# Performance work log

Hardware: AMD Instinct MI355X
Metric: run time of the kernel (lower is better)

The kernel has to match this reference:

```python
import jax, jax.numpy as jnp
import numpy as np

T, N = 8, 4096
F_IN, F1, F2 = 128, 128, 64


def _topk_summary(emb, p, k):
    # emb: [N, r], p: [r] random projection. Returns [r, k].
    scores = emb @ p / jnp.linalg.norm(p)            # [N]
    vals, idx = jax.lax.top_k(scores, k)             # N >= k always here
    return (emb[idx] * jnp.tanh(vals)[:, None]).T    # [r, k]


def _cell(W, U, B, prev_Q, feats, p):
    # GRU-style evolution of GCN weights. prev_Q: [r, c]; feats: [N, r].
    k = prev_Q.shape[1]
    z = _topk_summary(feats, p, k)                   # [r, c]
    wz = jnp.einsum('grs,sc->grc', W, z[None].repeat(3, 0)[0][None].squeeze(0)[None, ...].squeeze(0)[None].squeeze(0)) if False else jnp.einsum('grs,sc->grc', W, z)
    u = jax.nn.sigmoid(wz[0] + U[0] @ prev_Q + B[0])
    r = jax.nn.sigmoid(wz[1] + U[1] @ prev_Q + B[1])
    h = jnp.tanh(wz[2] + U[2] @ (r * prev_Q) + B[2])
    return (1.0 - u) * prev_Q + u * h


def _grcu(W, U, B, initW, adj, feats, ps, act):
    # Sequential weight evolution over T snapshots via scan.
    def step(Q, inp):
        a, f, p = inp
        Qn = _cell(W, U, B, Q, f, p)
        emb = act(a @ (f @ Qn))                      # [N, c]
        return Qn, emb
    _, out = jax.lax.scan(step, initW, (adj, feats, ps))
    return out                                       # [T, N, c]


def setup_inputs() -> dict:
    key = jax.random.key(0)
    ks = jax.random.split(key, 12)
    s_in = 1.0 / np.sqrt(F_IN)   # Gate init stdv (rows=128 for both layers)
    s1 = 1.0 / np.sqrt(F1)
    s2 = 1.0 / np.sqrt(F2)
    adj = jax.random.uniform(ks[0], (T, N, N), dtype=jnp.float32) / N  # ~row-normalized dense adjacency
    feats = jax.random.normal(ks[1], (T, N, F_IN), dtype=jnp.float32)
    return {
        'adj': adj,
        'feats': feats,
        'p1': jax.random.normal(ks[2], (T, F_IN), dtype=jnp.float32),
        'p2': jax.random.normal(ks[3], (T, F1), dtype=jnp.float32),
        'W1': jax.random.uniform(ks[4], (3, F_IN, F_IN), minval=-s_in, maxval=s_in, dtype=jnp.float32),
        'U1': jax.random.uniform(ks[5], (3, F_IN, F_IN), minval=-s_in, maxval=s_in, dtype=jnp.float32),
        'B1': jnp.zeros((3, F_IN, F1), dtype=jnp.float32),
        'initW1': jax.random.uniform(ks[6], (F_IN, F1), minval=-s1, maxval=s1, dtype=jnp.float32),
        'W2': jax.random.uniform(ks[7], (3, F1, F1), minval=-s1, maxval=s1, dtype=jnp.float32),
        'U2': jax.random.uniform(ks[8], (3, F1, F1), minval=-s1, maxval=s1, dtype=jnp.float32),
        'B2': jnp.zeros((3, F1, F2), dtype=jnp.float32),
        'initW2': jax.random.uniform(ks[9], (F1, F2), minval=-s2, maxval=s2, dtype=jnp.float32),
    }


def reference(adj, feats, p1, p2, W1, U1, B1, initW1, W2, U2, B2, initW2):
    h1 = _grcu(W1, U1, B1, initW1, adj, feats, p1, jax.nn.relu)   # [T, N, F1]
    h2 = _grcu(W2, U2, B2, initW2, adj, h1, p2, lambda x: x)      # [T, N, F2]
    return h2[-1]                                                 # [N, F2]
```

## Files before the change

kernel.cpp:

```cpp
#include <hip/hip_runtime.h>
#include <math.h>

#define TT 8
#define NN 4096
#define FF 128

typedef short bf16x8 __attribute__((ext_vector_type(8)));
typedef float f32x4 __attribute__((ext_vector_type(4)));

__device__ inline ushort f2bf(float f) {
  uint u = __float_as_uint(f);
  return (ushort)((u + 0x7fffu + ((u >> 16) & 1u)) >> 16);
}
__device__ inline float bf2f(ushort h) { return __uint_as_float(((uint)h) << 16); }

__device__ inline void split8(const float* v, uint4& H, uint4& L) {
  ushort h[8], l[8];
  #pragma unroll
  for (int j = 0; j < 8; ++j) {
    h[j] = f2bf(v[j]);
    l[j] = f2bf(v[j] - bf2f(h[j]));
  }
  H = make_uint4((uint)h[0] | ((uint)h[1] << 16), (uint)h[2] | ((uint)h[3] << 16),
                 (uint)h[4] | ((uint)h[5] << 16), (uint)h[6] | ((uint)h[7] << 16));
  L = make_uint4((uint)l[0] | ((uint)l[1] << 16), (uint)l[2] | ((uint)l[3] << 16),
                 (uint)l[4] | ((uint)l[5] << 16), (uint)l[6] | ((uint)l[7] << 16));
}

__global__ void norm_p_k(const float* __restrict__ p1, const float* __restrict__ p2,
                         float* __restrict__ pn1, float* __restrict__ pn2) {
  int b = blockIdx.x;
  int which = b >> 3, t = b & 7;
  const float* src = which ? p2 : p1;
  float* dst = which ? pn2 : pn1;
  int lane = threadIdx.x;
  float v0 = src[t*FF + lane];
  float v1 = src[t*FF + 64 + lane];
  float ss = v0*v0 + v1*v1;
  #pragma unroll
  for (int o = 32; o > 0; o >>= 1) ss += __shfl_xor(ss, o);
  float inv = 1.0f / sqrtf(ss);
  dst[t*FF + lane] = v0 * inv;
  dst[t*FF + 64 + lane] = v1 * inv;
}

__global__ __launch_bounds__(256)
void scores_k(const float* __restrict__ src, const float* __restrict__ pn,
              float* __restrict__ sc) {
  __shared__ float ps[FF];
  int t = blockIdx.y;
  int tid = threadIdx.x;
  if (tid < FF) ps[tid] = pn[t*FF + tid];
  __syncthreads();
  int row = blockIdx.x * 64 + (tid >> 2);
  int part = tid & 3;
  const float* rp = src + ((long)t*NN + row)*FF + part*32;
  float acc = 0.f;
  #pragma unroll
  for (int i = 0; i < 8; ++i) {
    float4 f = *reinterpret_cast<const float4*>(rp + i*4);
    const float* pp = ps + part*32 + i*4;
    acc += f.x*pp[0] + f.y*pp[1] + f.z*pp[2] + f.w*pp[3];
  }
  acc += __shfl_xor(acc, 1);
  acc += __shfl_xor(acc, 2);
  if (part == 0) sc[t*NN + row] = acc;
}

template<int K>
__global__ __launch_bounds__(1024)
void sortz_k(const float* __restrict__ sc, const float* __restrict__ src,
             float* __restrict__ z) {
  __shared__ float s[NN];
  __shared__ int  si[NN];
  __shared__ float tv[K];
  int t = blockIdx.x, tid = threadIdx.x;
  for (int i = tid; i < NN; i += 1024) { s[i] = sc[(long)t*NN + i]; si[i] = i; }
  __syncthreads();
  for (int k = 2; k <= NN; k <<= 1) {
    for (int j = k >> 1; j > 0; j >>= 1) {
      for (int i = tid; i < NN; i += 1024) {
        int l = i ^ j;
        if (l > i) {
          float a = s[i], b = s[l]; int ia = si[i], ib = si[l];
          bool dir = ((i & k) == 0);
          bool lp = (b > a) || (b == a && ib < ia);
          if (lp == dir) { s[i] = b; s[l] = a; si[i] = ib; si[l] = ia; }
        }
      }
      __syncthreads();
    }
  }
  if (tid < K) tv[tid] = tanhf(s[tid]);
  __syncthreads();
  for (int e = tid; e < FF*K; e += 1024) {
    int c = e >> 7, r = e & 127;
    z[((long)t*FF + r)*K + c] = src[((long)t*NN + si[c])*FF + r] * tv[c];
  }
}

template<int C>
__global__ __launch_bounds__(128)
void cell_k(const float* __restrict__ W, const float* __restrict__ U,
            const float* __restrict__ B, const float* __restrict__ z,
            const float* __restrict__ Qp, float* __restrict__ Qo) {
  __shared__ float zc[4][FF], qc[4][FF], rq[4][FF];
  int i = threadIdx.x;
  int j0 = blockIdx.x * 4;
  #pragma unroll
  for (int jj = 0; jj < 4; ++jj) {
    zc[jj][i] = z[i*C + j0 + jj];
    qc[jj][i] = Qp[i*C + j0 + jj];
  }
  __syncthreads();
  float a0[4] = {0,0,0,0}, a1[4] = {0,0,0,0};
  const float* W0 = W + i*FF;            const float* W1r = W + FF*FF + i*FF;
  const float* U0 = U + i*FF;            const float* U1r = U + FF*FF + i*FF;
  #pragma unroll 4
  for (int k = 0; k < FF; ++k) {
    float w0 = W0[k], w1 = W1r[k], u0 = U0[k], u1 = U1r[k];
    #pragma unroll
    for (int jj = 0; jj < 4; ++jj) {
      a0[jj] += w0*zc[jj][k] + u0*qc[jj][k];
      a1[jj] += w1*zc[jj][k] + u1*qc[jj][k];
    }
  }
  float uu[4];
  #pragma unroll
  for (int jj = 0; jj < 4; ++jj) {
    float xu = a0[jj] + B[0*FF*C + i*C + j0+jj];
    uu[jj] = 1.0f / (1.0f + expf(-xu));
    float xr = a1[jj] + B[1*FF*C + i*C + j0+jj];
    float r = 1.0f / (1.0f + expf(-xr));
    rq[jj][i] = r * qc[jj][i];
  }
  __syncthreads();
  float ah[4] = {0,0,0,0};
  const float* W2 = W + 2*FF*FF + i*FF;  const float* U2 = U + 2*FF*FF + i*FF;
  #pragma unroll 4
  for (int k = 0; k < FF; ++k) {
    float w2 = W2[k], u2 = U2[k];
    #pragma unroll
    for (int jj = 0; jj < 4; ++jj) ah[jj] += w2*zc[jj][k] + u2*rq[jj][k];
  }
  #pragma unroll
  for (int jj = 0; jj < 4; ++jj) {
    float h = tanhf(ah[jj] + B[2*FF*C + i*C + j0+jj]);
    float q = qc[jj][i];
    Qo[i*C + j0+jj] = (1.0f - uu[jj])*q + uu[jj]*h;
  }
}

__global__ __launch_bounds__(256)
void xmul_pack_k(const float* __restrict__ in, const float* __restrict__ Q,
                 ushort* __restrict__ Bph, ushort* __restrict__ Bpl) {
  constexpr int C = 128, RPT = 16;
  __shared__ float Qs[64*C];
  __shared__ float ft[FF][36];
  int t = blockIdx.y;
  const float* inT = in + (long)t*NN*FF;
  const float* QT  = Q  + (long)t*128*128;
  int tid = threadIdx.x;
  int r0 = blockIdx.x * 32;
  for (int v = tid; v < 32*FF/4; v += 256) {
    int row = v >> 5, kq = v & 31;
    float4 f = *reinterpret_cast<const float4*>(inT + ((long)(r0+row))*FF + kq*4);
    ft[kq*4+0][row] = f.x; ft[kq*4+1][row] = f.y;
    ft[kq*4+2][row] = f.z; ft[kq*4+3][row] = f.w;
  }
  int c = tid & (C-1);
  int rh = tid / C;
  float acc[RPT];
  #pragma unroll
  for (int r = 0; r < RPT; ++r) acc[r] = 0.f;
  for (int kc = 0; kc < 2; ++kc) {
    __syncthreads();
    for (int v = tid*4; v < 64*C; v += 1024)
      *reinterpret_cast<float4*>(&Qs[v]) =
        *reinterpret_cast<const float4*>(QT + kc*64*C + v);
    __syncthreads();
    #pragma unroll 8
    for (int kl = 0; kl < 64; ++kl) {
      int k = kc*64 + kl;
      float qv = Qs[kl*C + c];
      const float* fr = &ft[k][rh*RPT];
      #pragma unroll
      for (int r4 = 0; r4 < RPT/4; ++r4) {
        float4 fv = *reinterpret_cast<const float4*>(fr + r4*4);
        acc[r4*4+0] += fv.x*qv; acc[r4*4+1] += fv.y*qv;
        acc[r4*4+2] += fv.z*qv; acc[r4*4+3] += fv.w*qv;
      }
    }
  }
  #pragma unroll
  for (int g = 0; g < 2; ++g) {
    uint4 H, L;
    split8(&acc[g*8], H, L);
    long k0 = r0 + rh*16 + g*8;
    long off = ((long)t*512*128 + (k0 >> 3)*128 + c)*8;
    *reinterpret_cast<uint4*>(&Bph[off]) = H;
    *reinterpret_cast<uint4*>(&Bpl[off]) = L;
  }
}

__global__ __launch_bounds__(256)
void xmul_k64(const float* __restrict__ in, const float* __restrict__ Q,
              float* __restrict__ out) {
  constexpr int C = 64, RPT = 8;
  __shared__ float Qs[64*C];
  __shared__ float ft[FF][36];
  const float* inT = in;
  const float* QT  = Q;
  int tid = threadIdx.x;
  int r0 = blockIdx.x * 32;
  for (int v = tid; v < 32*FF/4; v += 256) {
    int row = v >> 5, kq = v & 31;
    float4 f = *reinterpret_cast<const float4*>(inT + ((long)(r0+row))*FF + kq*4);
    ft[kq*4+0][row] = f.x; ft[kq*4+1][row] = f.y;
    ft[kq*4+2][row] = f.z; ft[kq*4+3][row] = f.w;
  }
  int c = tid & (C-1);
  int rh = tid / C;
  float acc[RPT];
  #pragma unroll
  for (int r = 0; r < RPT; ++r) acc[r] = 0.f;
  for (int kc = 0; kc < 2; ++kc) {
    __syncthreads();
    for (int v = tid*4; v < 64*C; v += 1024)
      *reinterpret_cast<float4*>(&Qs[v]) =
        *reinterpret_cast<const float4*>(QT + kc*64*C + v);
    __syncthreads();
    #pragma unroll 8
    for (int kl = 0; kl < 64; ++kl) {
      int k = kc*64 + kl;
      float qv = Qs[kl*C + c];
      const float* fr = &ft[k][rh*RPT];
      #pragma unroll
      for (int r4 = 0; r4 < RPT/4; ++r4) {
        float4 fv = *reinterpret_cast<const float4*>(fr + r4*4);
        acc[r4*4+0] += fv.x*qv; acc[r4*4+1] += fv.y*qv;
        acc[r4*4+2] += fv.z*qv; acc[r4*4+3] += fv.w*qv;
      }
    }
  }
  #pragma unroll
  for (int r = 0; r < RPT; ++r)
    out[((long)(r0 + rh*RPT + r))*C + c] = acc[r];
}

#define ASTRIDE 40

__global__ __launch_bounds__(256, 2)
void gemm_mfma_k(const float* __restrict__ A, const ushort* __restrict__ Bph,
                 const ushort* __restrict__ Bpl, float* __restrict__ H) {
  __shared__ ushort AsH[2][64*ASTRIDE];
  __shared__ ushort AsL[2][64*ASTRIDE];
  int bid = blockIdx.x;
  int t = bid & 7, mb = bid >> 3;
  const float* At = A + (size_t)t*NN*NN + (size_t)mb*64*NN;
  const ushort* BhT = Bph + (size_t)t*512*128*8;
  const ushort* BlT = Bpl + (size_t)t*512*128*8;
  float* Ht = H + (size_t)t*NN*FF + (size_t)mb*64*FF;

  int tid = threadIdx.x;
  int wave = tid >> 6, lane = tid & 63;
  int lg = lane >> 4, lr = lane & 15;

  int srow = tid >> 2, skq = tid & 3;
  const float* aLoad = At + (size_t)srow*NN + skq*8;
  int sOff = srow*ASTRIDE + skq*8;

  int fOff = (16*wave + lr)*ASTRIDE + lg*8;

  size_t bOff = (size_t)lg*1024 + (size_t)lr*8;

  f32x4 acc[8];
  #pragma unroll
  for (int n = 0; n < 8; ++n) acc[n] = (f32x4){0.f, 0.f, 0.f, 0.f};

  {
    float4 a0 = *reinterpret_cast<const float4*>(aLoad);
    float4 a1 = *reinterpret_cast<const float4*>(aLoad + 4);
    float v[8] = {a0.x,a0.y,a0.z,a0.w,a1.x,a1.y,a1.z,a1.w};
    uint4 Hh, Ll; split8(v, Hh, Ll);
    *reinterpret_cast<uint4*>(&AsH[0][sOff]) = Hh;
    *reinterpret_cast<uint4*>(&AsL[0][sOff]) = Ll;
  }
  __syncthreads();

  for (int s = 0; s < 128; ++s) {
    int cur = s & 1;
    float4 a0, a1;
    if (s < 127) {
      a0 = *reinterpret_cast<const float4*>(aLoad + (s+1)*32);
      a1 = *reinterpret_cast<const float4*>(aLoad + (s+1)*32 + 4);
    }
    const ushort* bh = BhT + (size_t)s*4096 + bOff;
    const ushort* bl = BlT + (size_t)s*4096 + bOff;
    bf16x8 ah = *reinterpret_cast<const bf16x8*>(&AsH[cur][fOff]);
    bf16x8 al = *reinterpret_cast<const bf16x8*>(&AsL[cur][fOff]);
    #pragma unroll
    for (int n = 0; n < 8; ++n) {
      bf16x8 bhf = *reinterpret_cast<const bf16x8*>(bh + n*128);
      bf16x8 blf = *reinterpret_cast<const bf16x8*>(bl + n*128);
      acc[n] = __builtin_amdgcn_mfma_f32_16x16x32_bf16(ah, bhf, acc[n], 0, 0, 0);
      acc[n] = __builtin_amdgcn_mfma_f32_16x16x32_bf16(al, bhf, acc[n], 0, 0, 0);
      acc[n] = __builtin_amdgcn_mfma_f32_16x16x32_bf16(ah, blf, acc[n], 0, 0, 0);
    }
    if (s < 127) {
      float v[8] = {a0.x,a0.y,a0.z,a0.w,a1.x,a1.y,a1.z,a1.w};
      uint4 Hh, Ll; split8(v, Hh, Ll);
      *reinterpret_cast<uint4*>(&AsH[cur^1][sOff]) = Hh;
      *reinterpret_cast<uint4*>(&AsL[cur^1][sOff]) = Ll;
    }
    __syncthreads();
  }

  #pragma unroll
  for (int n = 0; n < 8; ++n)
    #pragma unroll
    for (int v = 0; v < 4; ++v)
      Ht[(size_t)(16*wave + lg*4 + v)*FF + 16*n + lr] = fmaxf(acc[n][v], 0.f);
}

__global__ __launch_bounds__(256, 2)
void gemm_adj64_k(const float* __restrict__ A, const float* __restrict__ X,
                  float* __restrict__ C_) {
  constexpr int BM = 64, KB = 32, BN = 64, TN = 4, XROW = 72;
  __shared__ float As[KB][BM+4];
  __shared__ float Xs[KB*XROW];
  const float* At = A;
  const float* Xt = X;
  float* Ct = C_;
  int brow = blockIdx.x * BM;
  int tid = threadIdx.x;
  int tr = tid >> 4, tc = tid & 15;
  int arow = tid & 63, aq = tid >> 6;
  int xkk = tid >> 3;
  int xcg = (tid & 7) * 8;

  float acc[4][TN];
  #pragma unroll
  for (int i = 0; i < 4; ++i)
    #pragma unroll
    for (int j = 0; j < TN; ++j) acc[i][j] = 0.f;

  float4 ar0, ar1, xr0, xr1;
  const float* aBase = At + ((long)(brow + arow))*NN;

  auto loadG = [&](int k0) {
    ar0 = *reinterpret_cast<const float4*>(aBase + k0 + aq*8);
    ar1 = *reinterpret_cast<const float4*>(aBase + k0 + aq*8 + 4);
    const float* xp = Xt + ((long)(k0 + xkk))*BN + xcg;
    xr0 = *reinterpret_cast<const float4*>(xp);
    xr1 = *reinterpret_cast<const float4*>(xp + 4);
  };
  auto storeL = [&]() {
    As[aq*8+0][arow] = ar0.x; As[aq*8+1][arow] = ar0.y;
    As[aq*8+2][arow] = ar0.z; As[aq*8+3][arow] = ar0.w;
    As[aq*8+4][arow] = ar1.x; As[aq*8+5][arow] = ar1.y;
    As[aq*8+6][arow] = ar1.z; As[aq*8+7][arow] = ar1.w;
    int base = xkk*XROW + xcg;
    *reinterpret_cast<float4*>(&Xs[base+0]) = xr0;
    *reinterpret_cast<float4*>(&Xs[base+4]) = xr1;
  };
  auto compute = [&]() {
    #pragma unroll 8
    for (int kk = 0; kk < KB; ++kk) {
      float4 av = *reinterpret_cast<const float4*>(&As[kk][tr*4]);
      float4 b0 = *reinterpret_cast<const float4*>(&Xs[kk*XROW + tc*4]);
      float xv[TN] = {b0.x, b0.y, b0.z, b0.w};
      float am[4] = {av.x, av.y, av.z, av.w};
      #pragma unroll
      for (int i = 0; i < 4; ++i)
        #pragma unroll
        for (int j = 0; j < TN; ++j)
          acc[i][j] += am[i]*xv[j];
    }
  };

  loadG(0);
  storeL();
  __syncthreads();
  for (int ch = 1; ch < NN/KB; ++ch) {
    loadG(ch*KB);
    compute();
    __syncthreads();
    storeL();
    __syncthreads();
  }
  compute();

  #pragma unroll
  for (int i = 0; i < 4; ++i) {
    int row = brow + tr*4 + i;
    float* op = Ct + (long)row*BN + tc*TN;
    float4 o;
    o.x = acc[i][0]; o.y = acc[i][1]; o.z = acc[i][2]; o.w = acc[i][3];
    *reinterpret_cast<float4*>(op) = o;
  }
}

extern "C" void kernel_launch(void* const* d_in, const int* in_sizes, int n_in,
                              void* d_out, int out_size, void* d_ws, size_t ws_size,
                              hipStream_t stream) {
  (void)in_sizes; (void)n_in; (void)out_size; (void)ws_size;
  const float* adj   = (const float*)d_in[0];
  const float* feats = (const float*)d_in[1];
  const float* p1    = (const float*)d_in[2];
  const float* p2    = (const float*)d_in[3];
  const float* W1    = (const float*)d_in[4];
  const float* U1    = (const float*)d_in[5];
  const float* B1    = (const float*)d_in[6];
  const float* iW1   = (const float*)d_in[7];
  const float* W2    = (const float*)d_in[8];
  const float* U2    = (const float*)d_in[9];
  const float* B2    = (const float*)d_in[10];
  const float* iW2   = (const float*)d_in[11];
  float* out = (float*)d_out;
  float* ws  = (float*)d_ws;

  const long NF = (long)NN*FF;
  ushort* Bph = (ushort*)ws;
  ushort* Bpl = (ushort*)(ws + 2097152);
  float* h1  = ws + 4194304;
  float* sc  = ws + 8388608;
  float* pn1 = ws + 8421376;
  float* pn2 = ws + 8422400;
  float* z1  = ws + 8423424;
  float* z2  = ws + 8554496;
  float* Q1  = ws + 8620032;
  float* Q2  = ws + 8751104;
  float* Y   = ws + 8816640;

  norm_p_k<<<16, 64, 0, stream>>>(p1, p2, pn1, pn2);

  scores_k<<<dim3(64,8), 256, 0, stream>>>(feats, pn1, sc);
  sortz_k<128><<<8, 1024, 0, stream>>>(sc, feats, z1);
  for (int t = 0; t < TT; ++t)
    cell_k<128><<<32, 128, 0, stream>>>(W1, U1, B1, z1 + (long)t*128*128,
                                        t ? Q1 + (long)(t-1)*128*128 : iW1,
                                        Q1 + (long)t*128*128);
  xmul_pack_k<<<dim3(128,8), 256, 0, stream>>>(feats, Q1, Bph, Bpl);
  gemm_mfma_k<<<512, 256, 0, stream>>>(adj, Bph, Bpl, h1);

  scores_k<<<dim3(64,8), 256, 0, stream>>>(h1, pn2, sc);
  sortz_k<64><<<8, 1024, 0, stream>>>(sc, h1, z2);
  for (int t = 0; t < TT; ++t)
    cell_k<64><<<16, 128, 0, stream>>>(W2, U2, B2, z2 + (long)t*128*64,
                                       t ? Q2 + (long)(t-1)*128*64 : iW2,
                                       Q2 + (long)t*128*64);
  xmul_k64<<<128, 256, 0, stream>>>(h1 + 7*NF, Q2 + (long)7*128*64, Y);
  gemm_adj64_k<<<64, 256, 0, stream>>>(adj + (long)7*NN*NN, Y, out);
}
```

Baseline: 1.715 ms.

## Fuse GRU cell steps into one kernel and use MFMA for final adjacency GEMM

```diff
diff --git a/kernel.cpp b/kernel.cpp
--- a/kernel.cpp
+++ b/kernel.cpp
@@ -99,67 +99,86 @@
   }
 }
 
+template<int C, bool WRITEALL>
+__global__ __launch_bounds__(256)
+void cells_k(const float* __restrict__ W, const float* __restrict__ U,
+             const float* __restrict__ B, const float* __restrict__ z,
+             const float* __restrict__ Q0, float* __restrict__ Qout) {
+  __shared__ float zc[128][16], Qc[128][16], rq[128][16];
+  int tid = threadIdx.x;
+  int jj = tid & 15, ig = tid >> 4;
+  int j0 = blockIdx.x * 16;
+  #pragma unroll
+  for (int p = 0; p < 8; ++p) {
+    int e = p*256 + tid; int i = e >> 4, c = e & 15;
+    Qc[i][c] = Q0[i*C + j0 + c];
+  }
+  __syncthreads();
+  for (int t = 0; t < TT; ++t) {
+    #pragma unroll
+    for (int p = 0; p < 8; ++p) {
+      int e = p*256 + tid; int i = e >> 4, c = e & 15;
+      zc[i][c] = z[((long)t*128 + i)*C + j0 + c];
+    }
+    __syncthreads();
+    float uu[8];
+    #pragma unroll
+    for (int rr = 0; rr < 8; ++rr) {
+      int i = ig*8 + rr;
+      float a0 = B[(0*128 + i)*C + j0 + jj];
+      float a1 = B[(1*128 + i)*C + j0 + jj];
+      const float* W0 = W + i*128;
+      const float* W1 = W + 128*128 + i*128;
+      const float* U0 = U + i*128;
+      const float* U1 = U + 128*128 + i*128;
+      #pragma unroll 4
+      for (int k = 0; k < 128; ++k) {
+        float zv = zc[k][jj], qv = Qc[k][jj];
+        a0 += W0[k]*zv + U0[k]*qv;
+        a1 += W1[k]*zv + U1[k]*qv;
+      }
+      float uv = 1.0f / (1.0f + expf(-a0));
+      float rv = 1.0f / (1.0f + expf(-a1));
+      uu[rr] = uv;
+      rq[i][jj] = rv * Qc[i][jj];
+    }
+    __syncthreads();
+    float qn[8];
+    #pragma unroll
+    for (int rr = 0; rr < 8; ++rr) {
+      int i = ig*8 + rr;
+      float ah = B[(2*128 + i)*C + j0 + jj];
+      const float* W2 = W + 2*128*128 + i*128;
+      const float* U2 = U + 2*128*128 + i*128;
+      #pragma unroll 4
+      for (int k = 0; k < 128; ++k)
+        ah += W2[k]*zc[k][jj] + U2[k]*rq[k][jj];
+      float hv = tanhf(ah);
+      qn[rr] = (1.0f - uu[rr])*Qc[i][jj] + uu[rr]*hv;
+    }
+    __syncthreads();
+    #pragma unroll
+    for (int rr = 0; rr < 8; ++rr) {
+      int i = ig*8 + rr;
+      Qc[i][jj] = qn[rr];
+      if (WRITEALL || t == TT-1)
+        Qout[((long)t*128 + i)*C + j0 + jj] = qn[rr];
+    }
+    __syncthreads();
+  }
+}
+
 template<int C>
-__global__ __launch_bounds__(128)
-void cell_k(const float* __restrict__ W, const float* __restrict__ U,
-            const float* __restrict__ B, const float* __restrict__ z,
-            const float* __restrict__ Qp, float* __restrict__ Qo) {
-  __shared__ float zc[4][FF], qc[4][FF], rq[4][FF];
-  int i = threadIdx.x;
-  int j0 = blockIdx.x * 4;
-  #pragma unroll
-  for (int jj = 0; jj < 4; ++jj) {
-    zc[jj][i] = z[i*C + j0 + jj];
-    qc[jj][i] = Qp[i*C + j0 + jj];
-  }
-  __syncthreads();
-  float a0[4] = {0,0,0,0}, a1[4] = {0,0,0,0};
-  const float* W0 = W + i*FF;            const float* W1r = W + FF*FF + i*FF;
-  const float* U0 = U + i*FF;            const float* U1r = U + FF*FF + i*FF;
-  #pragma unroll 4
-  for (int k = 0; k < FF; ++k) {
-    float w0 = W0[k], w1 = W1r[k], u0 = U0[k], u1 = U1r[k];
-    #pragma unroll
-    for (int jj = 0; jj < 4; ++jj) {
-      a0[jj] += w0*zc[jj][k] + u0*qc[jj][k];
-      a1[jj] += w1*zc[jj][k] + u1*qc[jj][k];
-    }
-  }
-  float uu[4];
-  #pragma unroll
-  for (int jj = 0; jj < 4; ++jj) {
-    float xu = a0[jj] + B[0*FF*C + i*C + j0+jj];
-    uu[jj] = 1.0f / (1.0f + expf(-xu));
-    float xr = a1[jj] + B[1*FF*C + i*C + j0+jj];
-    float r = 1.0f / (1.0f + expf(-xr));
-    rq[jj][i] = r * qc[jj][i];
-  }
-  __syncthreads();
-  float ah[4] = {0,0,0,0};
-  const float* W2 = W + 2*FF*FF + i*FF;  const float* U2 = U + 2*FF*FF + i*FF;
-  #pragma unroll 4
-  for (int k = 0; k < FF; ++k) {
-    float w2 = W2[k], u2 = U2[k];
-    #pragma unroll
-    for (int jj = 0; jj < 4; ++jj) ah[jj] += w2*zc[jj][k] + u2*rq[jj][k];
-  }
-  #pragma unroll
-  for (int jj = 0; jj < 4; ++jj) {
-    float h = tanhf(ah[jj] + B[2*FF*C + i*C + j0+jj]);
-    float q = qc[jj][i];
-    Qo[i*C + j0+jj] = (1.0f - uu[jj])*q + uu[jj]*h;
-  }
-}
-
 __global__ __launch_bounds__(256)
 void xmul_pack_k(const float* __restrict__ in, const float* __restrict__ Q,
-                 ushort* __restrict__ Bph, ushort* __restrict__ Bpl) {
-  constexpr int C = 128, RPT = 16;
+                 ushort* __restrict__ Bph, ushort* __restrict__ Bpl,
+                 long inST, long qST) {
+  constexpr int RPT = C / 8;
   __shared__ float Qs[64*C];
   __shared__ float ft[FF][36];
   int t = blockIdx.y;
-  const float* inT = in + (long)t*NN*FF;
-  const float* QT  = Q  + (long)t*128*128;
+  const float* inT = in + (long)t*inST;
+  const float* QT  = Q  + (long)t*qST;
   int tid = threadIdx.x;
   int r0 = blockIdx.x * 32;
   for (int v = tid; v < 32*FF/4; v += 256) {
@@ -193,212 +212,93 @@
     }
   }
   #pragma unroll
-  for (int g = 0; g < 2; ++g) {
+  for (int g = 0; g < RPT/8; ++g) {
     uint4 H, L;
     split8(&acc[g*8], H, L);
-    long k0 = r0 + rh*16 + g*8;
-    long off = ((long)t*512*128 + (k0 >> 3)*128 + c)*8;
+    long k0 = r0 + rh*RPT + g*8;
+    long off = ((long)t*512*C + (k0 >> 3)*C + c)*8;
     *reinterpret_cast<uint4*>(&Bph[off]) = H;
     *reinterpret_cast<uint4*>(&Bpl[off]) = L;
   }
 }
 
-__global__ __launch_bounds__(256)
-void xmul_k64(const float* __restrict__ in, const float* __restrict__ Q,
-              float* __restrict__ out) {
-  constexpr int C = 64, RPT = 8;
-  __shared__ float Qs[64*C];
-  __shared__ float ft[FF][36];
-  const float* inT = in;
-  const float* QT  = Q;
+template<int BN, int BM, bool RELU>
+__global__ __launch_bounds__((BM/16)*64, 2)
+void gemm_mfma_k(const float* __restrict__ A, const ushort* __restrict__ Bph,
+                 const ushort* __restrict__ Bpl, float* __restrict__ H, int nt) {
+  constexpr int TH = (BM/16)*64;
+  constexpr int NF = BN/16;
+  constexpr int BI = BN*64;
+  constexpr int NCH = BI/(TH*8);
+  __shared__ ushort BhL[BI];
+  __shared__ ushort BlL[BI];
+  int bid = blockIdx.x;
+  int t  = (nt == 8) ? (bid & 7) : 0;
+  int mb = (nt == 8) ? (bid >> 3) : bid;
+  const float*  At  = A   + (size_t)t*NN*NN + (size_t)mb*BM*NN;
+  const ushort* BhT = Bph + (size_t)t*512*BN*8;
+  const ushort* BlT = Bpl + (size_t)t*512*BN*8;
+  float* Ht = H + (size_t)t*NN*BN + (size_t)mb*BM*BN;
+
   int tid = threadIdx.x;
-  int r0 = blockIdx.x * 32;
-  for (int v = tid; v < 32*FF/4; v += 256) {
-    int row = v >> 5, kq = v & 31;
-    float4 f = *reinterpret_cast<const float4*>(inT + ((long)(r0+row))*FF + kq*4);
-    ft[kq*4+0][row] = f.x; ft[kq*4+1][row] = f.y;
-    ft[kq*4+2][row] = f.z; ft[kq*4+3][row] = f.w;
-  }
-  int c = tid & (C-1);
-  int rh = tid / C;
-  float acc[RPT];
-  #pragma unroll
-  for (int r = 0; r < RPT; ++r) acc[r] = 0.f;
-  for (int kc = 0; kc < 2; ++kc) {
-    __syncthreads();
-    for (int v = tid*4; v < 64*C; v += 1024)
-      *reinterpret_cast<float4*>(&Qs[v]) =
-        *reinterpret_cast<const float4*>(QT + kc*64*C + v);
-    __syncthreads();
-    #pragma unroll 8
-    for (int kl = 0; kl < 64; ++kl) {
-      int k = kc*64 + kl;
-      float qv = Qs[kl*C + c];
-      const float* fr = &ft[k][rh*RPT];
+  int wv = tid >> 6, lane = tid & 63;
+  int lg = lane >> 4, lr = lane & 15;
+
+  const float* aB = At + (size_t)(wv*16 + lr)*NN + lg*8;
+
+  f32x4 acc[NF];
+  #pragma unroll
+  for (int n = 0; n < NF; ++n) acc[n] = (f32x4){0.f, 0.f, 0.f, 0.f};
+
+  for (int iv = 0; iv < 64; ++iv) {
+    uint4 bb[NCH], cc[NCH];
+    const ushort* bhg = BhT + (size_t)iv*BI + tid*8;
+    const ushort* blg = BlT + (size_t)iv*BI + tid*8;
+    #pragma unroll
+    for (int ch = 0; ch < NCH; ++ch) {
+      bb[ch] = *reinterpret_cast<const uint4*>(bhg + ch*TH*8);
+      cc[ch] = *reinterpret_cast<const uint4*>(blg + ch*TH*8);
+    }
+    const float* ap = aB + (size_t)iv*64;
+    float4 a0 = *reinterpret_cast<const float4*>(ap);
+    float4 a1 = *reinterpret_cast<const float4*>(ap + 4);
+    float4 a2 = *reinterpret_cast<const float4*>(ap + 32);
+    float4 a3 = *reinterpret_cast<const float4*>(ap + 36);
+
+    __syncthreads();
+    #pragma unroll
+    for (int ch = 0; ch < NCH; ++ch) {
+      *reinterpret_cast<uint4*>(&BhL[tid*8 + ch*TH*8]) = bb[ch];
+      *reinterpret_cast<uint4*>(&BlL[tid*8 + ch*TH*8]) = cc[ch];
+    }
+    __syncthreads();
+
+    auto dohalf = [&](float4 x0, float4 x1, int ss) {
+      float v[8] = {x0.x, x0.y, x0.z, x0.w, x1.x, x1.y, x1.z, x1.w};
+      uint4 Hh, Ll; split8(v, Hh, Ll);
+      bf16x8 ah = *reinterpret_cast<bf16x8*>(&Hh);
+      bf16x8 al = *reinterpret_cast<bf16x8*>(&Ll);
+      int base = (ss*4 + lg)*BN*8 + lr*8;
       #pragma unroll
-      for (int r4 = 0; r4 < RPT/4; ++r4) {
-        float4 fv = *reinterpret_cast<const float4*>(fr + r4*4);
-        acc[r4*4+0] += fv.x*qv; acc[r4*4+1] += fv.y*qv;
-        acc[r4*4+2] += fv.z*qv; acc[r4*4+3] += fv.w*qv;
+      for (int n = 0; n < NF; ++n) {
+        bf16x8 bh = *reinterpret_cast<const bf16x8*>(&BhL[base + n*128]);
+        bf16x8 bl = *reinterpret_cast<const bf16x8*>(&BlL[base + n*128]);
+        acc[n] = __builtin_amdgcn_mfma_f32_16x16x32_bf16(ah, bh, acc[n], 0, 0, 0);
+        acc[n] = __builtin_amdgcn_mfma_f32_16x16x32_bf16(al, bh, acc[n], 0, 0, 0);
+        acc[n] = __builtin_amdgcn_mfma_f32_16x16x32_bf16(ah, bl, acc[n], 0, 0, 0);
       }
-    }
-  }
-  #pragma unroll
-  for (int r = 0; r < RPT; ++r)
-    out[((long)(r0 + rh*RPT + r))*C + c] = acc[r];
-}
-
-#define ASTRIDE 40
-
-__global__ __launch_bounds__(256, 2)
-void gemm_mfma_k(const float* __restrict__ A, const ushort* __restrict__ Bph,
-                 const ushort* __restrict__ Bpl, float* __restrict__ H) {
-  __shared__ ushort AsH[2][64*ASTRIDE];
-  __shared__ ushort AsL[2][64*ASTRIDE];
-  int bid = blockIdx.x;
-  int t = bid & 7, mb = bid >> 3;
-  const float* At = A + (size_t)t*NN*NN + (size_t)mb*64*NN;
-  const ushort* BhT = Bph + (size_t)t*512*128*8;
-  const ushort* BlT = Bpl + (size_t)t*512*128*8;
-  float* Ht = H + (size_t)t*NN*FF + (size_t)mb*64*FF;
-
-  int tid = threadIdx.x;
-  int wave = tid >> 6, lane = tid & 63;
-  int lg = lane >> 4, lr = lane & 15;
-
-  int srow = tid >> 2, skq = tid & 3;
-  const float* aLoad = At + (size_t)srow*NN + skq*8;
-  int sOff = srow*ASTRIDE + skq*8;
-
-  int fOff = (16*wave + lr)*ASTRIDE + lg*8;
-
-  size_t bOff = (size_t)lg*1024 + (size_t)lr*8;
-
-  f32x4 acc[8];
-  #pragma unroll
-  for (int n = 0; n < 8; ++n) acc[n] = (f32x4){0.f, 0.f, 0.f, 0.f};
-
-  {
-    float4 a0 = *reinterpret_cast<const float4*>(aLoad);
-    float4 a1 = *reinterpret_cast<const float4*>(aLoad + 4);
-    float v[8] = {a0.x,a0.y,a0.z,a0.w,a1.x,a1.y,a1.z,a1.w};
-    uint4 Hh, Ll; split8(v, Hh, Ll);
-    *reinterpret_cast<uint4*>(&AsH[0][sOff]) = Hh;
-    *reinterpret_cast<uint4*>(&AsL[0][sOff]) = Ll;
-  }
-  __syncthreads();
-
-  for (int s = 0; s < 128; ++s) {
-    int cur = s & 1;
-    float4 a0, a1;
-    if (s < 127) {
-      a0 = *reinterpret_cast<const float4*>(aLoad + (s+1)*32);
-      a1 = *reinterpret_cast<const float4*>(aLoad + (s+1)*32 + 4);
-    }
-    const ushort* bh = BhT + (size_t)s*4096 + bOff;
-    const ushort* bl = BlT + (size_t)s*4096 + bOff;
-    bf16x8 ah = *reinterpret_cast<const bf16x8*>(&AsH[cur][fOff]);
-    bf16x8 al = *reinterpret_cast<const bf16x8*>(&AsL[cur][fOff]);
-    #pragma unroll
-    for (int n = 0; n < 8; ++n) {
-      bf16x8 bhf = *reinterpret_cast<const bf16x8*>(bh + n*128);
-      bf16x8 blf = *reinterpret_cast<const bf16x8*>(bl + n*128);
-      acc[n] = __builtin_amdgcn_mfma_f32_16x16x32_bf16(ah, bhf, acc[n], 0, 0, 0);
-      acc[n] = __builtin_amdgcn_mfma_f32_16x16x32_bf16(al, bhf, acc[n], 0, 0, 0);
-      acc[n] = __builtin_amdgcn_mfma_f32_16x16x32_bf16(ah, blf, acc[n], 0, 0, 0);
-    }
-    if (s < 127) {
-      float v[8] = {a0.x,a0.y,a0.z,a0.w,a1.x,a1.y,a1.z,a1.w};
-      uint4 Hh, Ll; split8(v, Hh, Ll);
-      *reinterpret_cast<uint4*>(&AsH[cur^1][sOff]) = Hh;
-      *reinterpret_cast<uint4*>(&AsL[cur^1][sOff]) = Ll;
-    }
-    __syncthreads();
-  }
-
-  #pragma unroll
-  for (int n = 0; n < 8; ++n)
-    #pragma unroll
-    for (int v = 0; v < 4; ++v)
-      Ht[(size_t)(16*wave + lg*4 + v)*FF + 16*n + lr] = fmaxf(acc[n][v], 0.f);
-}
-
-__global__ __launch_bounds__(256, 2)
-void gemm_adj64_k(const float* __restrict__ A, const float* __restrict__ X,
-                  float* __restrict__ C_) {
-  constexpr int BM = 64, KB = 32, BN = 64, TN = 4, XROW = 72;
-  __shared__ float As[KB][BM+4];
-  __shared__ float Xs[KB*XROW];
-  const float* At = A;
-  const float* Xt = X;
-  float* Ct = C_;
-  int brow = blockIdx.x * BM;
-  int tid = threadIdx.x;
-  int tr = tid >> 4, tc = tid & 15;
-  int arow = tid & 63, aq = tid >> 6;
-  int xkk = tid >> 3;
-  int xcg = (tid & 7) * 8;
-
-  float acc[4][TN];
-  #pragma unroll
-  for (int i = 0; i < 4; ++i)
-    #pragma unroll
-    for (int j = 0; j < TN; ++j) acc[i][j] = 0.f;
-
-  float4 ar0, ar1, xr0, xr1;
-  const float* aBase = At + ((long)(brow + arow))*NN;
-
-  auto loadG = [&](int k0) {
-    ar0 = *reinterpret_cast<const float4*>(aBase + k0 + aq*8);
-    ar1 = *reinterpret_cast<const float4*>(aBase + k0 + aq*8 + 4);
-    const float* xp = Xt + ((long)(k0 + xkk))*BN + xcg;
-    xr0 = *reinterpret_cast<const float4*>(xp);
-    xr1 = *reinterpret_cast<const float4*>(xp + 4);
-  };
-  auto storeL = [&]() {
-    As[aq*8+0][arow] = ar0.x; As[aq*8+1][arow] = ar0.y;
-    As[aq*8+2][arow] = ar0.z; As[aq*8+3][arow] = ar0.w;
-    As[aq*8+4][arow] = ar1.x; As[aq*8+5][arow] = ar1.y;
-    As[aq*8+6][arow] = ar1.z; As[aq*8+7][arow] = ar1.w;
-    int base = xkk*XROW + xcg;
-    *reinterpret_cast<float4*>(&Xs[base+0]) = xr0;
-    *reinterpret_cast<float4*>(&Xs[base+4]) = xr1;
-  };
-  auto compute = [&]() {
-    #pragma unroll 8
-    for (int kk = 0; kk < KB; ++kk) {
-      float4 av = *reinterpret_cast<const float4*>(&As[kk][tr*4]);
-      float4 b0 = *reinterpret_cast<const float4*>(&Xs[kk*XROW + tc*4]);
-      float xv[TN] = {b0.x, b0.y, b0.z, b0.w};
-      float am[4] = {av.x, av.y, av.z, av.w};
-      #pragma unroll
-      for (int i = 0; i < 4; ++i)
-        #pragma unroll
-        for (int j = 0; j < TN; ++j)
-          acc[i][j] += am[i]*xv[j];
-    }
-  };
-
-  loadG(0);
-  storeL();
-  __syncthreads();
-  for (int ch = 1; ch < NN/KB; ++ch) {
-    loadG(ch*KB);
-    compute();
-    __syncthreads();
-    storeL();
-    __syncthreads();
-  }
-  compute();
-
-  #pragma unroll
-  for (int i = 0; i < 4; ++i) {
-    int row = brow + tr*4 + i;
-    float* op = Ct + (long)row*BN + tc*TN;
-    float4 o;
-    o.x = acc[i][0]; o.y = acc[i][1]; o.z = acc[i][2]; o.w = acc[i][3];
-    *reinterpret_cast<float4*>(op) = o;
-  }
+    };
+    dohalf(a0, a1, 0);
+    dohalf(a2, a3, 1);
+  }
+
+  #pragma unroll
+  for (int n = 0; n < NF; ++n)
+    #pragma unroll
+    for (int v = 0; v < 4; ++v) {
+      float x = acc[n][v];
+      Ht[(size_t)(16*wv + lg*4 + v)*BN + 16*n + lr] = RELU ? fmaxf(x, 0.f) : x;
+    }
 }
 
 extern "C" void kernel_launch(void* const* d_in, const int* in_sizes, int n_in,
@@ -420,7 +320,7 @@
   float* out = (float*)d_out;
   float* ws  = (float*)d_ws;
 
-  const long NF = (long)NN*FF;
+  const long NF_ = (long)NN*FF;
   ushort* Bph = (ushort*)ws;
   ushort* Bpl = (ushort*)(ws + 2097152);
   float* h1  = ws + 4194304;
@@ -431,25 +331,24 @@
   float* z2  = ws + 8554496;
   float* Q1  = ws + 8620032;
   float* Q2  = ws + 8751104;
-  float* Y   = ws + 8816640;
+  ushort* Yh = (ushort*)(ws + 8816640);
+  ushort* Yl = Yh + 262144;
 
   norm_p_k<<<16, 64, 0, stream>>>(p1, p2, pn1, pn2);
 
   scores_k<<<dim3(64,8), 256, 0, stream>>>(feats, pn1, sc);
   sortz_k<128><<<8, 1024, 0, stream>>>(sc, feats, z1);
-  for (int t = 0; t < TT; ++t)
-    cell_k<128><<<32, 128, 0, stream>>>(W1, U1, B1, z1 + (long)t*128*128,
-                                        t ? Q1 + (long)(t-1)*128*128 : iW1,
-                                        Q1 + (long)t*128*128);
-  xmul_pack_k<<<dim3(128,8), 256, 0, stream>>>(feats, Q1, Bph, Bpl);
-  gemm_mfma_k<<<512, 256, 0, stream>>>(adj, Bph, Bpl, h1);
+  cells_k<128, true><<<8, 256, 0, stream>>>(W1, U1, B1, z1, iW1, Q1);
+  xmul_pack_k<128><<<dim3(128,8), 256, 0, stream>>>(feats, Q1, Bph, Bpl,
+                                                    NF_, 128*128);
+  gemm_mfma_k<128,64,true><<<512, 256, 0, stream>>>(adj, Bph, Bpl, h1, 8);
 
   scores_k<<<dim3(64,8), 256, 0, stream>>>(h1, pn2, sc);
   sortz_k<64><<<8, 1024, 0, stream>>>(sc, h1, z2);
-  for (int t = 0; t < TT; ++t)
-    cell_k<64><<<16, 128, 0, stream>>>(W2, U2, B2, z2 + (long)t*128*64,
-                                       t ? Q2 + (long)(t-1)*128*64 : iW2,
-                                       Q2 + (long)t*128*64);
-  xmul_k64<<<128, 256, 0, stream>>>(h1 + 7*NF, Q2 + (long)7*128*64, Y);
-  gemm_adj64_k<<<64, 256, 0, stream>>>(adj + (long)7*NN*NN, Y, out);
-}
+  cells_k<64, false><<<4, 256, 0, stream>>>(W2, U2, B2, z2, iW2, Q2);
+  xmul_pack_k<64><<<dim3(128,1), 256, 0, stream>>>(h1 + 7*NF_,
+                                                   Q2 + (long)7*128*64,
+                                                   Yh, Yl, 0, 0);
+  gemm_mfma_k<64,32,false><<<128, 128, 0, stream>>>(adj + (size_t)7*NN*NN,
+                                                    Yh, Yl, out, 1);
+}
```

Measured after the change: 2.584 ms. +50.7%, slower.
